# Kernel tuning notes

Measured on AMD Instinct MI355X. Metric: run time of the kernel, lower is better.

Reference implementation:

```python
import jax, jax.numpy as jnp
import numpy as np
from jax import lax

B, C, P = 512, 1, 64
N_MEM = 32768
HID = 16


def _conv(x, w, b):
    # x: [B,Cin,H,W], w: [Cout,Cin,3,3]
    y = lax.conv_general_dilated(x, w, (1, 1), 'SAME',
                                 dimension_numbers=('NCHW', 'OIHW', 'NCHW'))
    return y + b[None, :, None, None]


def setup_inputs() -> dict:
    key = jax.random.key(0)
    ks = jax.random.split(key, 16)
    s = 0.05
    inp = {
        'noisy': jax.random.normal(ks[0], (B, C, P, P), jnp.float32),
        'mem_noise_bank': jax.random.normal(ks[1], (N_MEM, C, P, P), jnp.float32),
        'mem_clean_bank': jax.random.normal(ks[2], (N_MEM, C, P, P), jnp.float32),
        # frozen base denoiser (3-layer residual conv)
        'bw1': jax.random.normal(ks[3], (HID, C, 3, 3), jnp.float32) * s,
        'bb1': jnp.zeros((HID,), jnp.float32),
        'bw2': jax.random.normal(ks[4], (HID, HID, 3, 3), jnp.float32) * s,
        'bb2': jnp.zeros((HID,), jnp.float32),
        'bw3': jax.random.normal(ks[5], (C, HID, 3, 3), jnp.float32) * s,
        'bb3': jnp.zeros((C,), jnp.float32),
        # adapter convs (3*C -> HID -> HID -> C); torch zero-inits last conv,
        # we use small random weights so the output exercises the full path
        'aw1': jax.random.normal(ks[6], (HID, 3 * C, 3, 3), jnp.float32) * s,
        'ab1': jnp.zeros((HID,), jnp.float32),
        'aw2': jax.random.normal(ks[7], (HID, HID, 3, 3), jnp.float32) * s,
        'ab2': jnp.zeros((HID,), jnp.float32),
        'aw3': jax.random.normal(ks[8], (C, HID, 3, 3), jnp.float32) * s,
        'ab3': jnp.zeros((C,), jnp.float32),
    }
    return inp


def _base(noisy, bw1, bb1, bw2, bb2, bw3, bb3):
    h = jax.nn.relu(_conv(noisy, bw1, bb1))
    h = jax.nn.relu(_conv(h, bw2, bb2))
    return noisy - _conv(h, bw3, bb3)


def _select_memory(noisy, mem_noise_bank, mem_clean_bank):
    nf = noisy.reshape(B, -1)                  # [B, D]
    mf = mem_noise_bank.reshape(N_MEM, -1)     # [N, D]
    a2 = jnp.sum(nf * nf, axis=1, keepdims=True)   # [B,1]
    b2 = jnp.sum(mf * mf, axis=1)[None, :]         # [1,N]
    dists = a2 + b2 - 2.0 * (nf @ mf.T)            # [B,N]
    idx = jnp.argmin(dists, axis=1)                # [B]
    return mem_clean_bank[idx]                     # [B,C,P,P]


def reference(noisy, mem_noise_bank, mem_clean_bank,
              bw1, bb1, bw2, bb2, bw3, bb3,
              aw1, ab1, aw2, ab2, aw3, ab3):
    base_out = lax.stop_gradient(_base(noisy, bw1, bb1, bw2, bb2, bw3, bb3))
    mem_clean = lax.stop_gradient(
        _select_memory(noisy, mem_noise_bank, mem_clean_bank))
    x = jnp.concatenate([noisy, base_out, mem_clean], axis=1)  # [B,3C,P,P]
    h = jax.nn.relu(_conv(x, aw1, ab1))
    h = jax.nn.relu(_conv(h, aw2, ab2))
    delta = _conv(h, aw3, ab3)
    return base_out + delta
```

## Files before the change

### kernel.cpp

```cpp
#include <hip/hip_runtime.h>
#include <hip/hip_bf16.h>
#include <cstdint>

#define B_IMG 512
#define NMEM  32768
#define DD    4096
#define HID   16

typedef __attribute__((ext_vector_type(8))) short short8;
typedef __attribute__((ext_vector_type(4))) float f32x4;
typedef unsigned long long ull;

__device__ __forceinline__ void gload16(const void* g, const void* l) {
  __builtin_amdgcn_global_load_lds(
      (const __attribute__((address_space(1))) void*)g,
      (__attribute__((address_space(3))) void*)l, 16, 0, 0);
}

__device__ __forceinline__ ushort to_bf16u(float f) {
  uint32_t u = __float_as_uint(f);
  return (ushort)((u + 0x7fffu + ((u >> 16) & 1u)) >> 16);
}

__device__ __forceinline__ uint32_t cvtpk(float lo, float hi) {
  uint32_t r;
  asm("v_cvt_pk_bf16_f32 %0, %1, %2" : "=v"(r) : "v"(lo), "v"(hi));
  return r;
}

__global__ __launch_bounds__(256) void sqnorm_kernel(const float* __restrict__ x,
                                                     float* __restrict__ out) {
  const int row = blockIdx.x;
  const float4* p = reinterpret_cast<const float4*>(x + (size_t)row * DD);
  float s = 0.f;
#pragma unroll
  for (int j = 0; j < 4; ++j) {
    float4 v = p[threadIdx.x + 256 * j];
    s += v.x * v.x + v.y * v.y + v.z * v.z + v.w * v.w;
  }
#pragma unroll
  for (int o = 32; o > 0; o >>= 1) s += __shfl_down(s, o);
  __shared__ float ls[4];
  if ((threadIdx.x & 63) == 0) ls[threadIdx.x >> 6] = s;
  __syncthreads();
  if (threadIdx.x == 0) out[row] = (ls[0] + ls[1]) + (ls[2] + ls[3]);
}

__global__ __launch_bounds__(256) void split_hi_kernel(const float* __restrict__ x,
                                                       ushort* __restrict__ hi,
                                                       float* __restrict__ nrm) {
  const int row = blockIdx.x;
  const int t = threadIdx.x;
  const float4* p = reinterpret_cast<const float4*>(x + (size_t)row * DD);
  ushort4* ph = reinterpret_cast<ushort4*>(hi + (size_t)row * DD);
  float s = 0.f;
#pragma unroll
  for (int j = 0; j < 4; ++j) {
    float4 v = p[t + 256 * j];
    float vv[4] = {v.x, v.y, v.z, v.w};
    ushort4 h;
    ushort* hp = &h.x;
#pragma unroll
    for (int q = 0; q < 4; ++q) {
      float f = vv[q];
      s += f * f;
      hp[q] = to_bf16u(f);
    }
    ph[t + 256 * j] = h;
  }
#pragma unroll
  for (int o = 32; o > 0; o >>= 1) s += __shfl_down(s, o);
  __shared__ float ls[4];
  if ((t & 63) == 0) ls[t >> 6] = s;
  __syncthreads();
  if (t == 0) nrm[row] = (ls[0] + ls[1]) + (ls[2] + ls[3]);
}

__global__ __launch_bounds__(256) void dist1f_kernel(
    const ushort* __restrict__ Ah_g, const float* __restrict__ Bf,
    const float* __restrict__ a2, float* __restrict__ dists) {
  const int d = blockIdx.x;
  const int xcd = d & 7;
  const int rest = d >> 3;
  const int mb = rest & 3;
  const int nb = (rest >> 2) * 8 + xcd;
  const int m0 = mb * 128;
  const int n0 = nb * 128;

  __shared__ __align__(16) char la[16384];
  __shared__ __align__(16) char lbB[16384];
  __shared__ float b2loc[128];

  const int t = threadIdx.x;
  const int lane = t & 63;
  const int wid = t >> 6;
  const int wm = wid >> 1;
  const int wn = wid & 1;

  f32x4 acc[4][4];
#pragma unroll
  for (int mi = 0; mi < 4; ++mi)
#pragma unroll
    for (int ni = 0; ni < 4; ++ni) {
      f32x4 z = {0.f, 0.f, 0.f, 0.f};
      acc[mi][ni] = z;
    }

  const int r0 = t >> 2, g0 = t & 3;
  const int c0 = ((g0 ^ ((r0 >> 1) & 3)) << 3);
  const int r1 = 64 + r0;
  const int c1 = ((g0 ^ ((r1 >> 1) & 3)) << 3);
  const float* Bp0 = Bf + (size_t)(n0 + r0) * DD + c0;
  const float* Bp1 = Bf + (size_t)(n0 + r1) * DD + c1;
  float s0 = 0.f, s1 = 0.f;

  int arow[2], acol[2];
#pragma unroll
  for (int j = 0; j < 2; ++j) {
    const int e = (j * 256 + t) * 8;
    arow[j] = e >> 5;
    const int gpos = (e >> 3) & 3;
    acol[j] = ((gpos ^ ((arow[j] >> 1) & 3)) << 3);
  }

  for (int k0 = 0; k0 < DD; k0 += 64) {
#pragma unroll
    for (int h = 0; h < 2; ++h)
#pragma unroll
      for (int j = 0; j < 2; ++j)
        gload16(Ah_g + ((size_t)(m0 + arow[j]) * DD + k0 + h * 32 + acol[j]),
                la + h * 8192 + (j * 256 + t) * 16);
#pragma unroll
    for (int h = 0; h < 2; ++h) {
      float4 f00 = *(const float4*)(Bp0 + k0 + h * 32);
      float4 f01 = *(const float4*)(Bp0 + k0 + h * 32 + 4);
      float4 f10 = *(const float4*)(Bp1 + k0 + h * 32);
      float4 f11 = *(const float4*)(Bp1 + k0 + h * 32 + 4);
      s0 += f00.x * f00.x + f00.y * f00.y + f00.z * f00.z + f00.w * f00.w;
      s0 += f01.x * f01.x + f01.y * f01.y + f01.z * f01.z + f01.w * f01.w;
      s1 += f10.x * f10.x + f10.y * f10.y + f10.z * f10.z + f10.w * f10.w;
      s1 += f11.x * f11.x + f11.y * f11.y + f11.z * f11.z + f11.w * f11.w;
      uint4 p0, p1;
      p0.x = cvtpk(f00.x, f00.y); p0.y = cvtpk(f00.z, f00.w);
      p0.z = cvtpk(f01.x, f01.y); p0.w = cvtpk(f01.z, f01.w);
      p1.x = cvtpk(f10.x, f10.y); p1.y = cvtpk(f10.z, f10.w);
      p1.z = cvtpk(f11.x, f11.y); p1.w = cvtpk(f11.z, f11.w);
      *(uint4*)(lbB + h * 8192 + t * 16) = p0;
      *(uint4*)(lbB + h * 8192 + 4096 + t * 16) = p1;
    }
    __syncthreads();

#pragma unroll
    for (int h = 0; h < 2; ++h) {
      short8 ah[4];
#pragma unroll
      for (int mi = 0; mi < 4; ++mi) {
        const int r = wm * 64 + mi * 16 + (lane & 15);
        const int off = r * 64 + ((((lane >> 4) ^ (r >> 1)) & 3) << 4);
        ah[mi] = *(const short8*)(la + h * 8192 + off);
      }
#pragma unroll
      for (int ni = 0; ni < 4; ++ni) {
        const int r = wn * 64 + ni * 16 + (lane & 15);
        const int off = r * 64 + ((((lane >> 4) ^ (r >> 1)) & 3) << 4);
        short8 bh = *(const short8*)(lbB + h * 8192 + off);
#pragma unroll
        for (int mi = 0; mi < 4; ++mi)
          acc[mi][ni] = __builtin_amdgcn_mfma_f32_16x16x32_bf16(ah[mi], bh, acc[mi][ni], 0, 0, 0);
      }
    }
    __syncthreads();
  }

  s0 += __shfl_xor(s0, 1); s0 += __shfl_xor(s0, 2);
  s1 += __shfl_xor(s1, 1); s1 += __shfl_xor(s1, 2);
  if ((t & 3) == 0) { b2loc[r0] = s0; b2loc[r1] = s1; }
  __syncthreads();

#pragma unroll
  for (int mi = 0; mi < 4; ++mi)
#pragma unroll
    for (int j = 0; j < 4; ++j) {
      const int m = m0 + wm * 64 + mi * 16 + (lane >> 4) * 4 + j;
      const float a2v = a2[m];
#pragma unroll
      for (int ni = 0; ni < 4; ++ni) {
        const int nl = wn * 64 + ni * 16 + (lane & 15);
        dists[(size_t)m * NMEM + n0 + nl] = (a2v + b2loc[nl]) - 2.0f * acc[mi][ni][j];
      }
    }
}

#define MARGIN 4.0f
#define MAXC 64
#define NCH 4
#define CHW (NMEM / NCH)
__global__ __launch_bounds__(256) void refine_kernel(
    const float* __restrict__ dists, const float* __restrict__ A,
    const float* __restrict__ Bm, const float* __restrict__ a2,
    ull* __restrict__ best) {
  const int m = blockIdx.x;
  const int base = blockIdx.y * CHW;
  const int t = threadIdx.x;
  const int lane = t & 63, wid = t >> 6;
  const float4* r4 = reinterpret_cast<const float4*>(dists + (size_t)m * NMEM + base);

  float lmin = 3.4e38f;
  for (int i = t; i < CHW / 4; i += 256) {
    float4 v = r4[i];
    lmin = fminf(lmin, fminf(fminf(v.x, v.y), fminf(v.z, v.w)));
  }
#pragma unroll
  for (int o = 32; o > 0; o >>= 1) lmin = fminf(lmin, __shfl_down(lmin, o));
  __shared__ float ws4[4];
  __shared__ float red[4];
  __shared__ float red2[4];
  __shared__ int cnt;
  __shared__ int cand[MAXC];
  if (lane == 0) ws4[wid] = lmin;
  if (t == 0) cnt = 0;
  __syncthreads();
  const float thresh = fminf(fminf(ws4[0], ws4[1]), fminf(ws4[2], ws4[3])) + MARGIN;

  for (int i = t; i < CHW / 4; i += 256) {
    float4 v = r4[i];
    float vv[4] = {v.x, v.y, v.z, v.w};
#pragma unroll
    for (int q = 0; q < 4; ++q)
      if (vv[q] < thresh) {
        int c = atomicAdd(&cnt, 1);
        if (c < MAXC) cand[c] = base + i * 4 + q;
      }
  }
  __syncthreads();
  const int nc = min(cnt, MAXC);

  ull bkey = ~0ull;
  const float4* a4 = reinterpret_cast<const float4*>(A + (size_t)m * DD);
  for (int c = 0; c < nc; ++c) {
    const int n = cand[c];
    const float4* b4 = reinterpret_cast<const float4*>(Bm + (size_t)n * DD);
    float s = 0.f, s2 = 0.f;
    for (int i = t; i < DD / 4; i += 256) {
      float4 av = a4[i], bv = b4[i];
      s += av.x * bv.x + av.y * bv.y + av.z * bv.z + av.w * bv.w;
      s2 += bv.x * bv.x + bv.y * bv.y + bv.z * bv.z + bv.w * bv.w;
    }
#pragma unroll
    for (int o = 32; o > 0; o >>= 1) {
      s += __shfl_down(s, o);
      s2 += __shfl_down(s2, o);
    }
    if (lane == 0) { red[wid] = s; red2[wid] = s2; }
    __syncthreads();
    if (t == 0) {
      const float dot = (red[0] + red[1]) + (red[2] + red[3]);
      const float b2n = (red2[0] + red2[1]) + (red2[2] + red2[3]);
      const float dv = (a2[m] + b2n) - 2.0f * dot;
      const ull key = ((ull)__float_as_uint(dv) << 32) | (unsigned)n;
      if (key < bkey) bkey = key;
    }
    __syncthreads();
  }
  if (t == 0) atomicMin(&best[m], bkey);
}

__global__ __launch_bounds__(256) void dist_argmin_kernel(
    const float* __restrict__ A, const float* __restrict__ Bm,
    const float* __restrict__ a2, const float* __restrict__ b2,
    ull* __restrict__ best) {
  __shared__ float As[32][128];
  __shared__ float Bs[32][128];
  const int tid = threadIdx.x;
  const int m0 = blockIdx.y * 128;
  const int n0 = blockIdx.x * 128;
  const int tm = tid >> 4, tn = tid & 15;
  const int sr = tid >> 3;
  const int sc = (tid & 7) << 2;
  float acc[8][8];
#pragma unroll
  for (int i = 0; i < 8; ++i)
#pragma unroll
    for (int j = 0; j < 8; ++j) acc[i][j] = 0.f;
  for (int k0 = 0; k0 < DD; k0 += 32) {
    __syncthreads();
#pragma unroll
    for (int r = 0; r < 4; ++r) {
      const int row = sr + (r << 5);
      float4 va = *reinterpret_cast<const float4*>(&A[(size_t)(m0 + row) * DD + k0 + sc]);
      As[sc + 0][row] = va.x; As[sc + 1][row] = va.y;
      As[sc + 2][row] = va.z; As[sc + 3][row] = va.w;
      float4 vb = *reinterpret_cast<const float4*>(&Bm[(size_t)(n0 + row) * DD + k0 + sc]);
      Bs[sc + 0][row] = vb.x; Bs[sc + 1][row] = vb.y;
      Bs[sc + 2][row] = vb.z; Bs[sc + 3][row] = vb.w;
    }
    __syncthreads();
#pragma unroll 8
    for (int kk = 0; kk < 32; ++kk) {
      float4 a0 = *reinterpret_cast<const float4*>(&As[kk][tm * 8]);
      float4 a1 = *reinterpret_cast<const float4*>(&As[kk][tm * 8 + 4]);
      float4 b0 = *reinterpret_cast<const float4*>(&Bs[kk][tn * 8]);
      float4 b1 = *reinterpret_cast<const float4*>(&Bs[kk][tn * 8 + 4]);
      float a[8] = {a0.x, a0.y, a0.z, a0.w, a1.x, a1.y, a1.z, a1.w};
      float b[8] = {b0.x, b0.y, b0.z, b0.w, b1.x, b1.y, b1.z, b1.w};
#pragma unroll
      for (int i = 0; i < 8; ++i)
#pragma unroll
        for (int j = 0; j < 8; ++j) acc[i][j] += a[i] * b[j];
    }
  }
  __syncthreads();
  ull* red = reinterpret_cast<ull*>(&As[0][0]);
#pragma unroll
  for (int i = 0; i < 8; ++i) {
    const int m = m0 + tm * 8 + i;
    const float a2v = a2[m];
    float bd = 3.4e38f;
    int bn = 0;
#pragma unroll
    for (int j = 0; j < 8; ++j) {
      const int n = n0 + tn * 8 + j;
      const float dval = (a2v + b2[n]) - 2.0f * acc[i][j];
      if (dval < bd) { bd = dval; bn = n; }
    }
    red[(tm * 8 + i) * 16 + tn] = ((ull)__float_as_uint(bd) << 32) | (unsigned)bn;
  }
  __syncthreads();
  if (tid < 128) {
    ull k = red[tid * 16];
#pragma unroll
    for (int t2 = 1; t2 < 16; ++t2) {
      ull c = red[tid * 16 + t2];
      if (c < k) k = c;
    }
    atomicMin(&best[m0 + tid], k);
  }
}

__global__ __launch_bounds__(256) void wprep_kernel(
    const float* __restrict__ w1, const float* __restrict__ w2,
    const float* __restrict__ w3, int ncin,
    float* __restrict__ wt1, ushort* __restrict__ wh2, ushort* __restrict__ wl2,
    ushort* __restrict__ wh3, ushort* __restrict__ wl3) {
  const int i = blockIdx.x * 256 + threadIdx.x;
  const int n1 = ncin * 144;
  if (i < n1) {
    const int co = i & 15, r = i >> 4;
    const int ci = r / 9, kk = r % 9;
    wt1[(ci * 9 + kk) * 16 + co] = w1[(co * ncin + ci) * 9 + kk];
  } else if (i < n1 + 5120) {
    const int j = i - n1;
    const int which = j / 2560;
    const int jj = j % 2560;
    const int co = jj / 160, k = jj % 160;
    float f = 0.f;
    if (which == 0) {
      if (k < 144) f = w2[co * 144 + (k & 15) * 9 + (k >> 4)];
    } else {
      if (co == 0 && k < 144) f = w3[(k & 15) * 9 + (k >> 4)];
    }
    const ushort hb = to_bf16u(f);
    const float fl = f - __uint_as_float((uint32_t)hb << 16);
    ushort* dh = (which == 0) ? wh2 : wh3;
    ushort* dl = (which == 0) ? wl2 : wl3;
    dh[co * 160 + k] = hb;
    dl[co * 160 + k] = to_bf16u(fl);
  }
}

template <int NCIN>
__global__ __launch_bounds__(256, 4) void fused_conv3_kernel(
    const float* __restrict__ chan0, const float* __restrict__ chan1,
    const float* __restrict__ memC, const ull* __restrict__ best,
    const float* __restrict__ wt1, const float* __restrict__ b1v,
    const ushort* __restrict__ wh2, const ushort* __restrict__ wl2,
    const float* __restrict__ b2v,
    const ushort* __restrict__ wh3, const ushort* __restrict__ wl3,
    const float* __restrict__ b3v,
    const float* __restrict__ addend, float sign, float* __restrict__ outp) {
  constexpr int SIN_SZ = NCIN * 1600;
  constexpr int H1 = SIN_SZ;
  constexpr int H2 = H1 + 10368;
  constexpr int ZP = H2 + 10368;
  constexpr int W1 = ZP + 64;
  constexpr int SB = W1 + NCIN * 576;
  __shared__ __align__(16) char smem[SB + 128];
  float* sIn = (float*)smem;
  float* sW1 = (float*)(smem + W1);
  float* sB = (float*)(smem + SB);

  const int tid = threadIdx.x;
  const int lane = tid & 63, wid = tid >> 6;
  const int img = blockIdx.x / 25;
  const int t = blockIdx.x % 25;
  const int y0 = (t / 5) * 14, x0 = (t % 5) * 14;

  const float* cptr[NCIN];
  cptr[0] = chan0 + (size_t)img * DD;
  if (NCIN == 3) {
    cptr[1] = chan1 + (size_t)img * DD;
    cptr[2] = memC + (size_t)(unsigned)(best[img] & 0xffffffffull) * DD;
  }

  if (tid < 16) *(float*)(smem + ZP + tid * 4) = 0.f;
  for (int i = tid; i < NCIN * 144; i += 256) sW1[i] = wt1[i];
  if (tid < 16) sB[tid] = b1v[tid];
  else if (tid < 32) sB[tid] = b2v[tid - 16];
  for (int i = tid; i < NCIN * 400; i += 256) {
    const int ci = i / 400, r = i % 400, yy = r / 20, xx = r % 20;
    const int gy = y0 + yy - 3, gx = x0 + xx - 3;
    float v = 0.f;
    if (gy >= 0 && gy < 64 && gx >= 0 && gx < 64) v = cptr[ci][gy * 64 + gx];
    sIn[ci * 400 + yy * 20 + xx] = v;
  }
  __syncthreads();

  {
    const int p0 = tid;
    const int p1t = tid + 256;
    const bool has1 = (p1t < 324);
    const int p1 = has1 ? p1t : 0;
    const int y0p = p0 / 18, x0p = p0 % 18;
    const int y1p = p1 / 18, x1p = p1 % 18;
    const int gy0 = y0 + y0p - 2, gx0 = x0 + x0p - 2;
    const int gy1 = y0 + y1p - 2, gx1 = x0 + x1p - 2;
    const bool in0 = ((unsigned)gy0 < 64u) && ((unsigned)gx0 < 64u);
    const bool in1 = has1 && ((unsigned)gy1 < 64u) && ((unsigned)gx1 < 64u);

    float acc0[16], acc1[16];
#pragma unroll
    for (int co = 0; co < 16; ++co) {
      acc0[co] = sB[co];
      acc1[co] = sB[co];
    }
    int io0 = y0p * 20 + x0p;
    int io1 = y1p * 20 + x1p;
    int wo = 0;
    int dx = 0, dy = 0;
#pragma unroll 1
    for (int tk = 0; tk < NCIN * 9; ++tk) {
      const float v0 = sIn[io0];
      const float v1 = sIn[io1];
      const float4* wq = reinterpret_cast<const float4*>(sW1 + wo);
#pragma unroll
      for (int q = 0; q < 4; ++q) {
        float4 w = wq[q];
        acc0[4 * q + 0] += w.x * v0; acc1[4 * q + 0] += w.x * v1;
        acc0[4 * q + 1] += w.y * v0; acc1[4 * q + 1] += w.y * v1;
        acc0[4 * q + 2] += w.z * v0; acc1[4 * q + 2] += w.z * v1;
        acc0[4 * q + 3] += w.w * v0; acc1[4 * q + 3] += w.w * v1;
      }
      wo += 16;
      if (++dx == 3) {
        dx = 0;
        if (++dy == 3) { dy = 0; io0 += 358; io1 += 358; }
        else { io0 += 18; io1 += 18; }
      } else { io0 += 1; io1 += 1; }
    }
    short8 h0, h1v;
#pragma unroll
    for (int c = 0; c < 8; ++c) {
      h0[c] = (short)(in0 ? to_bf16u(fmaxf(acc0[c], 0.f)) : 0);
      h1v[c] = (short)(in0 ? to_bf16u(fmaxf(acc0[8 + c], 0.f)) : 0);
    }
    *(short8*)(smem + H1 + p0 * 16) = h0;
    *(short8*)(smem + H1 + 5184 + p0 * 16) = h1v;
    if (has1) {
#pragma unroll
      for (int c = 0; c < 8; ++c) {
        h0[c] = (short)(in1 ? to_bf16u(fmaxf(acc1[c], 0.f)) : 0);
        h1v[c] = (short)(in1 ? to_bf16u(fmaxf(acc1[8 + c], 0.f)) : 0);
      }
      *(short8*)(smem + H1 + p1 * 16) = h0;
      *(short8*)(smem + H1 + 5184 + p1 * 16) = h1v;
    }
  }
  __syncthreads();

  const int xn = lane & 15;
  const int xk = lane >> 4;
  f32x4 acc2[4];
#pragma unroll
  for (int g = 0; g < 4; ++g) { f32x4 z = {0.f, 0.f, 0.f, 0.f}; acc2[g] = z; }
#pragma unroll
  for (int kq = 0; kq < 5; ++kq) {
    const int k0 = kq * 32;
    const int we = xn * 160 + k0 + xk * 8;
    short8 ah = *(const short8*)(wh2 + we);
    short8 al = *(const short8*)(wl2 + we);
    const int kb = k0 + xk * 8;
    const int tap = kb >> 4, cih = (kb >> 3) & 1;
    const bool zp = (tap >= 9);
    const int dy = tap / 3, dx = tap % 3;
    const int bbase = H1 + cih * 5184 + ((dy * 18) + xn + dx) * 16;
#pragma unroll
    for (int g = 0; g < 4; ++g) {
      const int y = wid * 4 + g;
      const int boff = zp ? ZP : (bbase + y * 288);
      short8 b = *(const short8*)(smem + boff);
      acc2[g] = __builtin_amdgcn_mfma_f32_16x16x32_bf16(ah, b, acc2[g], 0, 0, 0);
      acc2[g] = __builtin_amdgcn_mfma_f32_16x16x32_bf16(al, b, acc2[g], 0, 0, 0);
    }
  }
#pragma unroll
  for (int g = 0; g < 4; ++g) {
    const int y = wid * 4 + g;
    const int gy = y0 + y - 1, gx = x0 + xn - 1;
    const bool inimg = ((unsigned)gy < 64u) && ((unsigned)gx < 64u);
#pragma unroll
    for (int j = 0; j < 4; ++j) {
      const int co = xk * 4 + j;
      const float v = inimg ? fmaxf(acc2[g][j] + sB[16 + co], 0.f) : 0.f;
      *(ushort*)(smem + H2 + (co >> 3) * 5184 + (y * 18 + xn) * 16 + (co & 7) * 2) =
          to_bf16u(v);
    }
  }
  __syncthreads();

  f32x4 acc3[4];
#pragma unroll
  for (int g = 0; g < 4; ++g) { f32x4 z = {0.f, 0.f, 0.f, 0.f}; acc3[g] = z; }
#pragma unroll
  for (int kq = 0; kq < 5; ++kq) {
    const int k0 = kq * 32;
    const int we = xn * 160 + k0 + xk * 8;
    short8 ah = *(const short8*)(wh3 + we);
    short8 al = *(const short8*)(wl3 + we);
    const int kb = k0 + xk * 8;
    const int tap = kb >> 4, cih = (kb >> 3) & 1;
    const bool zp = (tap >= 9);
    const int dy = tap / 3, dx = tap % 3;
    const int bbase = H2 + cih * 5184 + ((dy * 18) + xn + dx) * 16;
#pragma unroll
    for (int g = 0; g < 4; ++g) {
      const int y = wid * 4 + g;
      const int boff = zp ? ZP : (bbase + y * 288);
      short8 b = *(const short8*)(smem + boff);
      acc3[g] = __builtin_amdgcn_mfma_f32_16x16x32_bf16(ah, b, acc3[g], 0, 0, 0);
      acc3[g] = __builtin_amdgcn_mfma_f32_16x16x32_bf16(al, b, acc3[g], 0, 0, 0);
    }
  }
  if (xk == 0) {
#pragma unroll
    for (int g = 0; g < 4; ++g) {
      const int y = wid * 4 + g;
      const int gy = y0 + y, gx = x0 + xn;
      if (y < 14 && xn < 14 && gy < 64 && gx < 64) {
        const size_t o = (size_t)img * DD + gy * 64 + gx;
        outp[o] = addend[o] + sign * (acc3[g][0] + b3v[0]);
      }
    }
  }
}

extern "C" void kernel_launch(void* const* d_in, const int* in_sizes, int n_in,
                              void* d_out, int out_size, void* d_ws, size_t ws_size,
                              hipStream_t stream) {
  (void)in_sizes; (void)n_in; (void)out_size;
  const float* noisy = (const float*)d_in[0];
  const float* memN  = (const float*)d_in[1];
  const float* memC  = (const float*)d_in[2];
  const float* bw1 = (const float*)d_in[3];
  const float* bb1 = (const float*)d_in[4];
  const float* bw2 = (const float*)d_in[5];
  const float* bb2 = (const float*)d_in[6];
  const float* bw3 = (const float*)d_in[7];
  const float* bb3 = (const float*)d_in[8];
  const float* aw1 = (const float*)d_in[9];
  const float* ab1 = (const float*)d_in[10];
  const float* aw2 = (const float*)d_in[11];
  const float* ab2 = (const float*)d_in[12];
  const float* aw3 = (const float*)d_in[13];
  const float* ab3 = (const float*)d_in[14];
  float* out_f32 = (float*)d_out;

  char* ws = (char*)d_ws;
  size_t off = 0;
  auto take = [&](size_t bytes) -> char* {
    char* p = ws + off;
    off += (bytes + 255) & ~(size_t)255;
    return p;
  };
  float* b2 = (float*)take((size_t)NMEM * 4);
  float* a2 = (float*)take((size_t)B_IMG * 4);
  ull* best = (ull*)take((size_t)B_IMG * 8);
  float* base_out = (float*)take((size_t)B_IMG * DD * 4);
  float* wt1b = (float*)take(144 * 4);
  ushort* wh2b = (ushort*)take(2560 * 2);
  ushort* wl2b = (ushort*)take(2560 * 2);
  ushort* wh3b = (ushort*)take(2560 * 2);
  ushort* wl3b = (ushort*)take(2560 * 2);
  float* wt1a = (float*)take(432 * 4);
  ushort* wh2a = (ushort*)take(2560 * 2);
  ushort* wl2a = (ushort*)take(2560 * 2);
  ushort* wh3a = (ushort*)take(2560 * 2);
  ushort* wl3a = (ushort*)take(2560 * 2);
  const size_t off_common = off;

  ushort* Ah = (ushort*)take((size_t)B_IMG * DD * 2);
  float* dists = (float*)take((size_t)B_IMG * NMEM * 4);
  const bool use_mfma = (off + 1024) <= ws_size;
  if (!use_mfma) off = off_common;

  wprep_kernel<<<21, 256, 0, stream>>>(bw1, bw2, bw3, 1, wt1b, wh2b, wl2b, wh3b, wl3b);
  wprep_kernel<<<22, 256, 0, stream>>>(aw1, aw2, aw3, 3, wt1a, wh2a, wl2a, wh3a, wl3a);

  hipMemsetAsync(best, 0xFF, (size_t)B_IMG * 8, stream);
  if (use_mfma) {
    split_hi_kernel<<<B_IMG, 256, 0, stream>>>(noisy, Ah, a2);
    dist1f_kernel<<<(NMEM / 128) * (B_IMG / 128), 256, 0, stream>>>(
        Ah, memN, a2, dists);
    refine_kernel<<<dim3(B_IMG, NCH), 256, 0, stream>>>(dists, noisy, memN, a2, best);
  } else {
    sqnorm_kernel<<<NMEM, 256, 0, stream>>>(memN, b2);
    sqnorm_kernel<<<B_IMG, 256, 0, stream>>>(noisy, a2);
    dist_argmin_kernel<<<dim3(NMEM / 128, B_IMG / 128), 256, 0, stream>>>(
        noisy, memN, a2, b2, best);
  }

  fused_conv3_kernel<1><<<B_IMG * 25, 256, 0, stream>>>(
      noisy, nullptr, nullptr, nullptr,
      wt1b, bb1, wh2b, wl2b, bb2, wh3b, wl3b, bb3, noisy, -1.0f, base_out);
  fused_conv3_kernel<3><<<B_IMG * 25, 256, 0, stream>>>(
      noisy, base_out, memC, best,
      wt1a, ab1, wh2a, wl2a, ab2, wh3a, wl3a, ab3, base_out, 1.0f, out_f32);
}
```

Baseline: 526.4 us.

## Fuse per-block distance minima into GEMM epilogue to shrink refine scan

The distance GEMM epilogue now computes a per-row minimum key over each 128-column tile and stores it with atomicMin into a blockmin buffer. The refine kernel reads those 256 tile minima per row to form the threshold, then rescans only the tiles whose minimum falls under the threshold, instead of two full passes over the 128 MB distance matrix. The cost is shuffles and atomics in the GEMM epilogue plus an extra memset. Each thread of the refine kernel also scans its 128 values serially, so accesses to those rows are uncoalesced.

```diff
diff --git a/kernel.cpp b/kernel.cpp
--- a/kernel.cpp
+++ b/kernel.cpp
@@ -78,7 +78,8 @@
 
 __global__ __launch_bounds__(256) void dist1f_kernel(
     const ushort* __restrict__ Ah_g, const float* __restrict__ Bf,
-    const float* __restrict__ a2, float* __restrict__ dists) {
+    const float* __restrict__ a2, float* __restrict__ dists,
+    ull* __restrict__ blockmin) {
   const int d = blockIdx.x;
   const int xcd = d & 7;
   const int rest = d >> 3;
@@ -183,54 +184,58 @@
     for (int j = 0; j < 4; ++j) {
       const int m = m0 + wm * 64 + mi * 16 + (lane >> 4) * 4 + j;
       const float a2v = a2[m];
+      ull rk = ~0ull;
 #pragma unroll
       for (int ni = 0; ni < 4; ++ni) {
         const int nl = wn * 64 + ni * 16 + (lane & 15);
-        dists[(size_t)m * NMEM + n0 + nl] = (a2v + b2loc[nl]) - 2.0f * acc[mi][ni][j];
-      }
+        const float dv = (a2v + b2loc[nl]) - 2.0f * acc[mi][ni][j];
+        dists[(size_t)m * NMEM + n0 + nl] = dv;
+        const ull key = ((ull)__float_as_uint(dv) << 32) | (unsigned)(n0 + nl);
+        if (key < rk) rk = key;
+      }
+#pragma unroll
+      for (int msk = 1; msk < 16; msk <<= 1) {
+        ull o = __shfl_xor(rk, msk);
+        if (o < rk) rk = o;
+      }
+      if ((lane & 15) == 0) atomicMin(&blockmin[(size_t)m * 256 + (n0 >> 7)], rk);
     }
 }
 
 #define MARGIN 4.0f
 #define MAXC 64
-#define NCH 4
-#define CHW (NMEM / NCH)
 __global__ __launch_bounds__(256) void refine_kernel(
-    const float* __restrict__ dists, const float* __restrict__ A,
-    const float* __restrict__ Bm, const float* __restrict__ a2,
-    ull* __restrict__ best) {
+    const float* __restrict__ dists, const ull* __restrict__ blockmin,
+    const float* __restrict__ A, const float* __restrict__ Bm,
+    const float* __restrict__ a2, ull* __restrict__ best) {
   const int m = blockIdx.x;
-  const int base = blockIdx.y * CHW;
   const int t = threadIdx.x;
   const int lane = t & 63, wid = t >> 6;
-  const float4* r4 = reinterpret_cast<const float4*>(dists + (size_t)m * NMEM + base);
-
-  float lmin = 3.4e38f;
-  for (int i = t; i < CHW / 4; i += 256) {
-    float4 v = r4[i];
-    lmin = fminf(lmin, fminf(fminf(v.x, v.y), fminf(v.z, v.w)));
-  }
-#pragma unroll
-  for (int o = 32; o > 0; o >>= 1) lmin = fminf(lmin, __shfl_down(lmin, o));
   __shared__ float ws4[4];
   __shared__ float red[4];
   __shared__ float red2[4];
   __shared__ int cnt;
   __shared__ int cand[MAXC];
+
+  const ull bk = blockmin[(size_t)m * 256 + t];
+  const float kv = __uint_as_float((uint32_t)(bk >> 32));
+  float lmin = kv;
+#pragma unroll
+  for (int o = 32; o > 0; o >>= 1) lmin = fminf(lmin, __shfl_down(lmin, o));
   if (lane == 0) ws4[wid] = lmin;
   if (t == 0) cnt = 0;
   __syncthreads();
   const float thresh = fminf(fminf(ws4[0], ws4[1]), fminf(ws4[2], ws4[3])) + MARGIN;
 
-  for (int i = t; i < CHW / 4; i += 256) {
-    float4 v = r4[i];
-    float vv[4] = {v.x, v.y, v.z, v.w};
-#pragma unroll
-    for (int q = 0; q < 4; ++q)
-      if (vv[q] < thresh) {
+  if (kv < thresh) {
+    const float* row = dists + (size_t)m * NMEM + t * 128;
+    for (int i = 0; i < 128; ++i) {
+      const float v = row[i];
+      if (v < thresh) {
         int c = atomicAdd(&cnt, 1);
-        if (c < MAXC) cand[c] = base + i * 4 + q;
-      }
+        if (c < MAXC) cand[c] = t * 128 + i;
+      }
+    }
   }
   __syncthreads();
   const int nc = min(cnt, MAXC);
@@ -599,6 +604,7 @@
 
   ushort* Ah = (ushort*)take((size_t)B_IMG * DD * 2);
   float* dists = (float*)take((size_t)B_IMG * NMEM * 4);
+  ull* blockmin = (ull*)take((size_t)B_IMG * 256 * 8);
   const bool use_mfma = (off + 1024) <= ws_size;
   if (!use_mfma) off = off_common;
 
@@ -607,10 +613,11 @@
 
   hipMemsetAsync(best, 0xFF, (size_t)B_IMG * 8, stream);
   if (use_mfma) {
+    hipMemsetAsync(blockmin, 0xFF, (size_t)B_IMG * 256 * 8, stream);
     split_hi_kernel<<<B_IMG, 256, 0, stream>>>(noisy, Ah, a2);
     dist1f_kernel<<<(NMEM / 128) * (B_IMG / 128), 256, 0, stream>>>(
-        Ah, memN, a2, dists);
-    refine_kernel<<<dim3(B_IMG, NCH), 256, 0, stream>>>(dists, noisy, memN, a2, best);
+        Ah, memN, a2, dists, blockmin);
+    refine_kernel<<<B_IMG, 256, 0, stream>>>(dists, blockmin, noisy, memN, a2, best);
   } else {
     sqnorm_kernel<<<NMEM, 256, 0, stream>>>(memN, b2);
     sqnorm_kernel<<<B_IMG, 256, 0, stream>>>(noisy, a2);
```

Result: slower. 539.8 us (+2.6%).
